# Optimization experiments

Hardware: AMD Instinct MI355X
Metric: run time of the kernel (lower is better)

Reference implementation:

```python
import jax, jax.numpy as jnp
import numpy as np

D_MODEL = 1024
NHEAD = 16
D_HEAD = D_MODEL // NHEAD


def setup_inputs() -> dict:
    key = jax.random.key(0)
    ks = jax.random.split(key, 5)
    s_in = 1.0 / np.sqrt(D_MODEL)
    x = jax.random.normal(ks[0], (2, 2048, D_MODEL), dtype=jnp.float32)
    Wqkv = jax.random.uniform(ks[1], (D_MODEL, 3 * D_MODEL), jnp.float32, -s_in, s_in)
    bqkv = jax.random.uniform(ks[2], (3 * D_MODEL,), jnp.float32, -s_in, s_in)
    Wproj = jax.random.uniform(ks[3], (D_MODEL, D_MODEL), jnp.float32, -s_in, s_in)
    bproj = jax.random.uniform(ks[4], (D_MODEL,), jnp.float32, -s_in, s_in)
    return {"x": x, "Wqkv": Wqkv, "bqkv": bqkv, "Wproj": Wproj, "bproj": bproj}


def reference(x, Wqkv, bqkv, Wproj, bproj):
    B, N, D = x.shape
    qkv = x @ Wqkv + bqkv                       # [B, N, 3D]
    q, k, v = jnp.split(qkv, 3, axis=-1)
    # [B, N, D] -> [B, H, N, d]
    def to_heads(t):
        return t.reshape(B, N, NHEAD, D_HEAD).transpose(0, 2, 1, 3)
    q, k, v = to_heads(q), to_heads(k), to_heads(v)
    scale = 1.0 / np.sqrt(D_HEAD).astype(np.float32)
    attn = jnp.einsum('bhqd,bhkd->bhqk', q, k) * scale
    attn = jax.nn.softmax(attn, axis=-1)
    y = jnp.einsum('bhqk,bhkd->bhqd', attn, v)  # [B, H, N, d]
    y = y.transpose(0, 2, 1, 3).reshape(B, N, D)
    return y @ Wproj + bproj
```

## Files before the change

kernel.cpp:

```cpp
#include <hip/hip_runtime.h>
#include <hip/hip_bf16.h>
#include <stdint.h>

typedef __hip_bfloat16 bf16;
typedef __attribute__((ext_vector_type(8))) short short8;
typedef __attribute__((ext_vector_type(4))) float f32x4;

#define QSCALE 0.18033688011f

__device__ __forceinline__ float fast_exp2(float x) {
#if __has_builtin(__builtin_amdgcn_exp2f)
  return __builtin_amdgcn_exp2f(x);
#else
  return exp2f(x);
#endif
}

__device__ __forceinline__ uint32_t pack2_bf16(float a, float b) {
#if __has_builtin(__builtin_amdgcn_cvt_pk_bf16_f32)
  typedef __attribute__((ext_vector_type(2))) __bf16 bf16x2;
  bf16x2 v = __builtin_amdgcn_cvt_pk_bf16_f32(a, b);
  return __builtin_bit_cast(uint32_t, v);
#else
  uint32_t ua = __builtin_bit_cast(uint32_t, a);
  uint32_t ub = __builtin_bit_cast(uint32_t, b);
  ua += 0x7FFF + ((ua >> 16) & 1);
  ub += 0x7FFF + ((ub >> 16) & 1);
  return (ua >> 16) | (ub & 0xFFFF0000u);
#endif
}

__device__ __forceinline__ void gload_lds16(const bf16* g, bf16* l) {
#if __has_builtin(__builtin_amdgcn_global_load_lds)
  __builtin_amdgcn_global_load_lds(
      (const __attribute__((address_space(1))) void*)(uintptr_t)g,
      (__attribute__((address_space(3))) void*)(uint32_t)(uintptr_t)l,
      16, 0, 0);
#else
  int lane = threadIdx.x & 63;
  *(short8*)(l + lane * 8) = *(const short8*)(g + lane * 8);
#endif
}

__device__ __forceinline__ void lds_barrier() {
  asm volatile("s_waitcnt lgkmcnt(0)\n\ts_barrier" ::: "memory");
}

__device__ __forceinline__ void transpose_tile(const float* __restrict__ in,
                                               bf16* __restrict__ out,
                                               int R, int C, int bx, int by,
                                               bf16 (*t)[72]) {
  const int r0 = by * 64, c0 = bx * 64;
  const int rr = threadIdx.x >> 3, cc = (threadIdx.x & 7) * 8;
#pragma unroll
  for (int rep = 0; rep < 2; ++rep) {
    int y = rr + rep * 32;
    const float* p = in + (size_t)(r0 + y) * C + c0 + cc;
    f32x4 v0 = *(const f32x4*)p;
    f32x4 v1 = *(const f32x4*)(p + 4);
#pragma unroll
    for (int j = 0; j < 4; ++j) {
      t[cc + j][y] = __float2bfloat16(v0[j]);
      t[cc + 4 + j][y] = __float2bfloat16(v1[j]);
    }
  }
  __syncthreads();
#pragma unroll
  for (int rep = 0; rep < 2; ++rep) {
    int y = rr + rep * 32;
    short8 v = *(const short8*)&t[y][cc];
    *(short8*)(out + (size_t)(c0 + y) * R + r0 + cc) = v;
  }
}

__global__ __launch_bounds__(256)
void prep_k(const float* __restrict__ x, bf16* __restrict__ xb,
            const float* __restrict__ Wqkv, bf16* __restrict__ WtQkv,
            const float* __restrict__ Wproj, bf16* __restrict__ WtP) {
  __shared__ __align__(16) bf16 t[64][72];
  const int bid = blockIdx.x;
  if (bid < 2048) {
    int i = (bid * 256 + threadIdx.x) * 8;
    f32x4 v0 = *(const f32x4*)(x + i);
    f32x4 v1 = *(const f32x4*)(x + i + 4);
    short8 r;
    bf16* rb = (bf16*)&r;
#pragma unroll
    for (int j = 0; j < 4; ++j) {
      rb[j] = __float2bfloat16(v0[j]);
      rb[4 + j] = __float2bfloat16(v1[j]);
    }
    *(short8*)(xb + i) = r;
  } else if (bid < 2048 + 768) {
    int b = bid - 2048;
    transpose_tile(Wqkv, WtQkv, 1024, 3072, b % 48, b / 48, t);
  } else {
    int b = bid - 2816;
    transpose_tile(Wproj, WtP, 1024, 1024, b % 16, b / 16, t);
  }
}

template <int MODE, int TM>
__global__ __launch_bounds__(256, 2)
void gemm_bt(const bf16* __restrict__ A, const bf16* __restrict__ Bt,
             const float* __restrict__ bias, float* __restrict__ outp,
             bf16* __restrict__ Qd, bf16* __restrict__ Kd, bf16* __restrict__ Vt,
             int M, int Nn, int K) {
  constexpr int MI = TM / 32;
  __shared__ __align__(16) bf16 smem[(TM == 128) ? 9216 : 6144];
  bf16* As = smem;
  bf16* Bs = smem + TM * 32;

  const int tid = threadIdx.x;
  const int wave = tid >> 6, lane = tid & 63;
  const int quad = lane >> 4, l16 = lane & 15;
  const int mw = (wave >> 1) * (TM / 2), nw = (wave & 1) * 64;
  const int m_blk = blockIdx.y * TM, n_blk = blockIdx.x * 128;

  f32x4 acc[MI][4];
#pragma unroll
  for (int i = 0; i < MI; ++i)
#pragma unroll
    for (int j = 0; j < 4; ++j) acc[i][j] = (f32x4){0.f, 0.f, 0.f, 0.f};

  const int rowA = lane >> 2, colA = (lane & 3) * 8;
  const int chunkB = wave * 2;
  const bf16* gB = Bt + (size_t)(n_blk + chunkB * 16 + rowA) * K + colA;
  bf16* lB0 = &Bs[chunkB * 16 * 32];
  bf16* lB1 = &Bs[(chunkB + 1) * 16 * 32];

  const int chunkA = (TM == 128) ? wave * 2 : wave;
  const bf16* gA = A + (size_t)(m_blk + chunkA * 16 + rowA) * K + colA;
  bf16* lA0 = &As[chunkA * 16 * 32];
  bf16* lA1 = &As[(chunkA + 1) * 16 * 32];

  for (int kt = 0; kt < K; kt += 32) {
    gload_lds16(gA, lA0);
    if (TM == 128) gload_lds16(gA + 16 * K, lA1);
    gload_lds16(gB, lB0);
    gload_lds16(gB + 16 * K, lB1);
    gA += 32; gB += 32;
    __syncthreads();
    short8 af[MI], bfv[4];
#pragma unroll
    for (int i = 0; i < MI; ++i)
      af[i] = *(const short8*)&As[(mw + i * 16 + l16) * 32 + quad * 8];
#pragma unroll
    for (int j = 0; j < 4; ++j)
      bfv[j] = *(const short8*)&Bs[(nw + j * 16 + l16) * 32 + quad * 8];
#pragma unroll
    for (int i = 0; i < MI; ++i)
#pragma unroll
      for (int j = 0; j < 4; ++j)
        acc[i][j] = __builtin_amdgcn_mfma_f32_16x16x32_bf16(af[i], bfv[j],
                                                            acc[i][j], 0, 0, 0);
    __syncthreads();
  }

  if (MODE == 0) {
    float bval[4];
#pragma unroll
    for (int j = 0; j < 4; ++j) bval[j] = bias[n_blk + nw + j * 16 + l16];

    const int part = n_blk >> 10;
    const int b = m_blk >> 11;
    const int tloc = m_blk & 2047;
    const int h0 = (n_blk & 1023) >> 6;

#pragma unroll
    for (int p = 0; p < 2; ++p) {
      __syncthreads();
      if ((nw >> 6) == p) {
        if (part == 2) {
#pragma unroll
          for (int i = 0; i < MI; ++i)
#pragma unroll
            for (int j = 0; j < 4; ++j) {
              const int dh = j * 16 + l16;
              const int t0 = mw + i * 16 + quad * 4;
              uint2 pk;
              pk.x = pack2_bf16(acc[i][j][0] + bval[j], acc[i][j][1] + bval[j]);
              pk.y = pack2_bf16(acc[i][j][2] + bval[j], acc[i][j][3] + bval[j]);
              *(uint2*)&smem[dh * 136 + t0] = pk;
            }
        } else {
          const float sc = (part == 0) ? QSCALE : 1.0f;
#pragma unroll
          for (int i = 0; i < MI; ++i)
#pragma unroll
            for (int j = 0; j < 4; ++j) {
              const int d = j * 16 + l16;
              const int t0 = mw + i * 16 + quad * 4;
#pragma unroll
              for (int r = 0; r < 4; ++r)
                smem[(t0 + r) * 72 + d] =
                    __float2bfloat16((acc[i][j][r] + bval[j]) * sc);
            }
        }
      }
      __syncthreads();
      const size_t bh = (size_t)(b * 16 + h0 + p);
      if (part == 2) {
#pragma unroll
        for (int it = 0; it < 4; ++it) {
          const int dl = (tid >> 4) + it * 16;
          const int t8 = (tid & 15) * 8;
          short8 v = *(const short8*)&smem[dl * 136 + t8];
          *(short8*)&Vt[(bh * 64 + dl) * 2048 + tloc + t8] = v;
        }
      } else {
        bf16* dst = (part == 0) ? Qd : Kd;
#pragma unroll
        for (int it = 0; it < 4; ++it) {
          const int row = (tid >> 3) + it * 32;
          const int col8 = (tid & 7) * 8;
          short8 v = *(const short8*)&smem[row * 72 + col8];
          *(short8*)&dst[(bh * 2048 + tloc + row) * 64 + col8] = v;
        }
      }
    }
  } else {
#pragma unroll
    for (int j = 0; j < 4; ++j) {
      const int ncol = n_blk + nw + j * 16 + l16;
      const float bval = bias[ncol];
#pragma unroll
      for (int i = 0; i < MI; ++i) {
        const int mrow0 = m_blk + mw + i * 16 + quad * 4;
#pragma unroll
        for (int r = 0; r < 4; ++r)
          outp[(size_t)(mrow0 + r) * Nn + ncol] = acc[i][j][r] + bval;
      }
    }
  }
}

__global__ __launch_bounds__(256, 4)
void attn_kernel(const bf16* __restrict__ Qg, const bf16* __restrict__ Kg,
                 const bf16* __restrict__ Vt, bf16* __restrict__ yg) {
  __shared__ __align__(16) bf16 Ks[64][72];
  __shared__ __align__(16) bf16 Vts[2][64 * 72];
  __shared__ __align__(16) bf16 Ps[64][72];

  const int tid = threadIdx.x;
  const int wave = tid >> 6, lane = tid & 63;
  const int quad = lane >> 4, l16 = lane & 15;
  const int qh = wave & 1, kvh = wave >> 1;

  const int bx = blockIdx.x;
  const int qt = bx & 31;
  const int bh = bx >> 5;

  const bf16* Qb = Qg + ((size_t)bh * 2048 + qt * 64) * 64;
  const bf16* Kb = Kg + (size_t)bh * 2048 * 64;
  const bf16* Vtb = Vt + (size_t)bh * 64 * 2048;

  short8 qf[2][2];
#pragma unroll
  for (int qblk = 0; qblk < 2; ++qblk)
#pragma unroll
    for (int kb = 0; kb < 2; ++kb)
      qf[qblk][kb] = *(const short8*)(
          Qb + (size_t)(qh * 32 + qblk * 16 + l16) * 64 + kb * 32 + quad * 8);

  f32x4 yacc[2][4];
#pragma unroll
  for (int qblk = 0; qblk < 2; ++qblk)
#pragma unroll
    for (int dblk = 0; dblk < 4; ++dblk)
      yacc[qblk][dblk] = (f32x4){0.f, 0.f, 0.f, 0.f};
  float sum_l[2] = {0.f, 0.f};

  const int kr = tid >> 3, kc = (tid & 7) * 8;
  const int vdd = tid & 63, vo = tid >> 6;
  const int voff0 = vdd * 72 + (((vo) + (vdd >> 3)) & 7) * 8;
  const int voff1 = vdd * 72 + (((vo + 4) + (vdd >> 3)) & 7) * 8;
  const bf16* Kp0 = Kb + (size_t)kr * 64 + kc;
  const bf16* Kp1 = Kb + (size_t)(kr + 32) * 64 + kc;
  const bf16* Vp0 = Vtb + (size_t)vdd * 2048 + vo * 8;
  const bf16* Vp1 = Vtb + (size_t)vdd * 2048 + (vo + 4) * 8;

  {
    short8 a = *(const short8*)Kp0;
    short8 b = *(const short8*)Kp1;
    short8 c = *(const short8*)Vp0;
    short8 d = *(const short8*)Vp1;
    *(short8*)&Ks[kr][kc] = a;
    *(short8*)&Ks[kr + 32][kc] = b;
    *(short8*)&Vts[0][voff0] = c;
    *(short8*)&Vts[0][voff1] = d;
  }
  short8 gk0 = *(const short8*)(Kp0 + (size_t)64 * 64);
  short8 gk1 = *(const short8*)(Kp1 + (size_t)64 * 64);
  short8 gv0 = *(const short8*)(Vp0 + 64);
  short8 gv1 = *(const short8*)(Vp1 + 64);
  __syncthreads();

  for (int kt = 0; kt < 2048; kt += 64) {
    const int cur = (kt >> 6) & 1;

    if (kt + 64 < 2048) {
      *(short8*)&Vts[cur ^ 1][voff0] = gv0;
      *(short8*)&Vts[cur ^ 1][voff1] = gv1;
      if (kt + 128 < 2048) {
        gv0 = *(const short8*)(Vp0 + kt + 128);
        gv1 = *(const short8*)(Vp1 + kt + 128);
      }
    }

    f32x4 st[2][2];
#pragma unroll
    for (int kvblk = 0; kvblk < 2; ++kvblk) {
      const int krow = kvh * 32 + kvblk * 16 + l16;
      short8 kf0 = *(const short8*)&Ks[krow][quad * 8];
      short8 kf1 = *(const short8*)&Ks[krow][32 + quad * 8];
#pragma unroll
      for (int qblk = 0; qblk < 2; ++qblk) {
        f32x4 a = (f32x4){0.f, 0.f, 0.f, 0.f};
        a = __builtin_amdgcn_mfma_f32_16x16x32_bf16(kf0, qf[qblk][0], a, 0, 0, 0);
        a = __builtin_amdgcn_mfma_f32_16x16x32_bf16(kf1, qf[qblk][1], a, 0, 0, 0);
        st[qblk][kvblk] = a;
      }
    }

#pragma unroll
    for (int qblk = 0; qblk < 2; ++qblk) {
      float ssum = 0.f;
#pragma unroll
      for (int kvblk = 0; kvblk < 2; ++kvblk) {
        float p0 = fast_exp2(st[qblk][kvblk][0]);
        float p1 = fast_exp2(st[qblk][kvblk][1]);
        float p2 = fast_exp2(st[qblk][kvblk][2]);
        float p3 = fast_exp2(st[qblk][kvblk][3]);
        ssum += (p0 + p1) + (p2 + p3);
        uint2 pk;
        pk.x = pack2_bf16(p0, p1);
        pk.y = pack2_bf16(p2, p3);
        *(uint2*)&Ps[qh * 32 + qblk * 16 + l16]
                    [kvh * 32 + kvblk * 16 + quad * 4] = pk;
      }
      sum_l[qblk] += ssum;
    }

    lds_barrier();

    if (kt + 64 < 2048) {
      *(short8*)&Ks[kr][kc] = gk0;
      *(short8*)&Ks[kr + 32][kc] = gk1;
      if (kt + 128 < 2048) {
        gk0 = *(const short8*)(Kp0 + (size_t)(kt + 128) * 64);
        gk1 = *(const short8*)(Kp1 + (size_t)(kt + 128) * 64);
      }
    }

    short8 vbf[4];
#pragma unroll
    for (int dblk = 0; dblk < 4; ++dblk) {
      const int d = dblk * 16 + l16;
      vbf[dblk] = *(const short8*)&Vts[cur][d * 72 +
          (((kvh * 4 + quad) + (d >> 3)) & 7) * 8];
    }
#pragma unroll
    for (int qblk = 0; qblk < 2; ++qblk) {
      short8 pa = *(const short8*)&Ps[qh * 32 + qblk * 16 + l16]
                                     [kvh * 32 + quad * 8];
#pragma unroll
      for (int dblk = 0; dblk < 4; ++dblk)
        yacc[qblk][dblk] = __builtin_amdgcn_mfma_f32_16x16x32_bf16(
            pa, vbf[dblk], yacc[qblk][dblk], 0, 0, 0);
    }

    lds_barrier();
  }

#pragma unroll
  for (int qblk = 0; qblk < 2; ++qblk) {
    sum_l[qblk] += __shfl_xor(sum_l[qblk], 16);
    sum_l[qblk] += __shfl_xor(sum_l[qblk], 32);
  }
  __syncthreads();
  float* red = (float*)&Vts[0][0];
  float* sred = (float*)&Ps[0][0];
  if (kvh == 1) {
#pragma unroll
    for (int qblk = 0; qblk < 2; ++qblk) {
#pragma unroll
      for (int dblk = 0; dblk < 4; ++dblk) {
        const int f = (qh * 2 + qblk) * 4 + dblk;
        *(f32x4*)&red[(f * 64 + quad * 16 + l16) * 4] = yacc[qblk][dblk];
      }
      if (quad == 0) sred[(qh * 2 + qblk) * 16 + l16] = sum_l[qblk];
    }
  }
  __syncthreads();
  if (kvh == 0) {
    const int b = bh >> 4, h = bh & 15;
    const size_t rowbase = (size_t)b * 2048 + qt * 64;
#pragma unroll
    for (int qblk = 0; qblk < 2; ++qblk) {
      sum_l[qblk] += sred[(qh * 2 + qblk) * 16 + l16];
#pragma unroll
      for (int dblk = 0; dblk < 4; ++dblk) {
        const int f = (qh * 2 + qblk) * 4 + dblk;
        f32x4 o = *(const f32x4*)&red[(f * 64 + quad * 16 + l16) * 4];
#pragma unroll
        for (int r = 0; r < 4; ++r) yacc[qblk][dblk][r] += o[r];
      }
#pragma unroll
      for (int r = 0; r < 4; ++r) {
        const float lv = __shfl(sum_l[qblk], quad * 4 + r, 16);
        const float inv = 1.f / lv;
        const int rr = qh * 32 + qblk * 16 + quad * 4 + r;
#pragma unroll
        for (int dblk = 0; dblk < 4; ++dblk)
          yg[(rowbase + rr) * 1024 + h * 64 + dblk * 16 + l16] =
              __float2bfloat16(yacc[qblk][dblk][r] * inv);
      }
    }
  }
}

extern "C" void kernel_launch(void* const* d_in, const int* in_sizes, int n_in,
                              void* d_out, int out_size, void* d_ws, size_t ws_size,
                              hipStream_t stream) {
  const float* x = (const float*)d_in[0];
  const float* Wqkv = (const float*)d_in[1];
  const float* bqkv = (const float*)d_in[2];
  const float* Wproj = (const float*)d_in[3];
  const float* bproj = (const float*)d_in[4];
  float* out = (float*)d_out;

  if (ws_size < (size_t)40 * 1024 * 1024) return;

  char* ws = (char*)d_ws;
  bf16* xb    = (bf16*)(ws + 0);
  bf16* yd    = (bf16*)(ws + 0);
  bf16* WtQkv = (bf16*)(ws + 8388608);
  bf16* WtP   = (bf16*)(ws + 14680064);
  bf16* Qd    = (bf16*)(ws + 16777216);
  bf16* Kd    = (bf16*)(ws + 25165824);
  bf16* Vten  = (bf16*)(ws + 33554432);

  prep_k<<<3072, 256, 0, stream>>>(x, xb, Wqkv, WtQkv, Wproj, WtP);
  gemm_bt<0, 128><<<dim3(24, 32), 256, 0, stream>>>(
      xb, WtQkv, bqkv, nullptr, Qd, Kd, Vten, 4096, 3072, 1024);
  attn_kernel<<<dim3(1024), 256, 0, stream>>>(Qd, Kd, Vten, yd);
  gemm_bt<1, 64><<<dim3(8, 64), 256, 0, stream>>>(
      yd, WtP, bproj, out, nullptr, nullptr, nullptr, 4096, 1024, 1024);
}
```

Measured before the change: 193.6 us.

## Load K/V MFMA fragments directly from global into registers, dropping LDS staging

```diff
diff --git a/kernel.cpp b/kernel.cpp
--- a/kernel.cpp
+++ b/kernel.cpp
@@ -42,10 +42,6 @@
 #endif
 }
 
-__device__ __forceinline__ void lds_barrier() {
-  asm volatile("s_waitcnt lgkmcnt(0)\n\ts_barrier" ::: "memory");
-}
-
 __device__ __forceinline__ void transpose_tile(const float* __restrict__ in,
                                                bf16* __restrict__ out,
                                                int R, int C, int bx, int by,
@@ -238,9 +234,8 @@
 __global__ __launch_bounds__(256, 4)
 void attn_kernel(const bf16* __restrict__ Qg, const bf16* __restrict__ Kg,
                  const bf16* __restrict__ Vt, bf16* __restrict__ yg) {
-  __shared__ __align__(16) bf16 Ks[64][72];
-  __shared__ __align__(16) bf16 Vts[2][64 * 72];
-  __shared__ __align__(16) bf16 Ps[64][72];
+  __shared__ __align__(16) char lds_pool[16640];
+  bf16 (*Ps)[72] = (bf16 (*)[72])lds_pool;
 
   const int tid = threadIdx.x;
   const int wave = tid >> 6, lane = tid & 63;
@@ -252,8 +247,8 @@
   const int bh = bx >> 5;
 
   const bf16* Qb = Qg + ((size_t)bh * 2048 + qt * 64) * 64;
-  const bf16* Kb = Kg + (size_t)bh * 2048 * 64;
-  const bf16* Vtb = Vt + (size_t)bh * 64 * 2048;
+  const bf16* kp = Kg + ((size_t)bh * 2048 + kvh * 32 + l16) * 64 + quad * 8;
+  const bf16* vp = Vt + ((size_t)bh * 64 + l16) * 2048 + kvh * 32 + quad * 8;
 
   short8 qf[2][2];
 #pragma unroll
@@ -263,6 +258,16 @@
       qf[qblk][kb] = *(const short8*)(
           Qb + (size_t)(qh * 32 + qblk * 16 + l16) * 64 + kb * 32 + quad * 8);
 
+  short8 kf[2][2], vf[4];
+#pragma unroll
+  for (int kvblk = 0; kvblk < 2; ++kvblk)
+#pragma unroll
+    for (int ks = 0; ks < 2; ++ks)
+      kf[kvblk][ks] = *(const short8*)(kp + kvblk * 1024 + ks * 32);
+#pragma unroll
+  for (int dblk = 0; dblk < 4; ++dblk)
+    vf[dblk] = *(const short8*)(vp + (size_t)dblk * 16 * 2048);
+
   f32x4 yacc[2][4];
 #pragma unroll
   for (int qblk = 0; qblk < 2; ++qblk)
@@ -271,56 +276,27 @@
       yacc[qblk][dblk] = (f32x4){0.f, 0.f, 0.f, 0.f};
   float sum_l[2] = {0.f, 0.f};
 
-  const int kr = tid >> 3, kc = (tid & 7) * 8;
-  const int vdd = tid & 63, vo = tid >> 6;
-  const int voff0 = vdd * 72 + (((vo) + (vdd >> 3)) & 7) * 8;
-  const int voff1 = vdd * 72 + (((vo + 4) + (vdd >> 3)) & 7) * 8;
-  const bf16* Kp0 = Kb + (size_t)kr * 64 + kc;
-  const bf16* Kp1 = Kb + (size_t)(kr + 32) * 64 + kc;
-  const bf16* Vp0 = Vtb + (size_t)vdd * 2048 + vo * 8;
-  const bf16* Vp1 = Vtb + (size_t)vdd * 2048 + (vo + 4) * 8;
-
-  {
-    short8 a = *(const short8*)Kp0;
-    short8 b = *(const short8*)Kp1;
-    short8 c = *(const short8*)Vp0;
-    short8 d = *(const short8*)Vp1;
-    *(short8*)&Ks[kr][kc] = a;
-    *(short8*)&Ks[kr + 32][kc] = b;
-    *(short8*)&Vts[0][voff0] = c;
-    *(short8*)&Vts[0][voff1] = d;
-  }
-  short8 gk0 = *(const short8*)(Kp0 + (size_t)64 * 64);
-  short8 gk1 = *(const short8*)(Kp1 + (size_t)64 * 64);
-  short8 gv0 = *(const short8*)(Vp0 + 64);
-  short8 gv1 = *(const short8*)(Vp1 + 64);
-  __syncthreads();
-
   for (int kt = 0; kt < 2048; kt += 64) {
-    const int cur = (kt >> 6) & 1;
-
-    if (kt + 64 < 2048) {
-      *(short8*)&Vts[cur ^ 1][voff0] = gv0;
-      *(short8*)&Vts[cur ^ 1][voff1] = gv1;
-      if (kt + 128 < 2048) {
-        gv0 = *(const short8*)(Vp0 + kt + 128);
-        gv1 = *(const short8*)(Vp1 + kt + 128);
-      }
-    }
-
     f32x4 st[2][2];
 #pragma unroll
-    for (int kvblk = 0; kvblk < 2; ++kvblk) {
-      const int krow = kvh * 32 + kvblk * 16 + l16;
-      short8 kf0 = *(const short8*)&Ks[krow][quad * 8];
-      short8 kf1 = *(const short8*)&Ks[krow][32 + quad * 8];
+    for (int kvblk = 0; kvblk < 2; ++kvblk)
 #pragma unroll
       for (int qblk = 0; qblk < 2; ++qblk) {
         f32x4 a = (f32x4){0.f, 0.f, 0.f, 0.f};
-        a = __builtin_amdgcn_mfma_f32_16x16x32_bf16(kf0, qf[qblk][0], a, 0, 0, 0);
-        a = __builtin_amdgcn_mfma_f32_16x16x32_bf16(kf1, qf[qblk][1], a, 0, 0, 0);
+        a = __builtin_amdgcn_mfma_f32_16x16x32_bf16(kf[kvblk][0], qf[qblk][0],
+                                                    a, 0, 0, 0);
+        a = __builtin_amdgcn_mfma_f32_16x16x32_bf16(kf[kvblk][1], qf[qblk][1],
+                                                    a, 0, 0, 0);
         st[qblk][kvblk] = a;
       }
+
+    if (kt + 64 < 2048) {
+      kp += 64 * 64;
+#pragma unroll
+      for (int kvblk = 0; kvblk < 2; ++kvblk)
+#pragma unroll
+        for (int ks = 0; ks < 2; ++ks)
+          kf[kvblk][ks] = *(const short8*)(kp + kvblk * 1024 + ks * 32);
     }
 
 #pragma unroll
@@ -342,24 +318,6 @@
       sum_l[qblk] += ssum;
     }
 
-    lds_barrier();
-
-    if (kt + 64 < 2048) {
-      *(short8*)&Ks[kr][kc] = gk0;
-      *(short8*)&Ks[kr + 32][kc] = gk1;
-      if (kt + 128 < 2048) {
-        gk0 = *(const short8*)(Kp0 + (size_t)(kt + 128) * 64);
-        gk1 = *(const short8*)(Kp1 + (size_t)(kt + 128) * 64);
-      }
-    }
-
-    short8 vbf[4];
-#pragma unroll
-    for (int dblk = 0; dblk < 4; ++dblk) {
-      const int d = dblk * 16 + l16;
-      vbf[dblk] = *(const short8*)&Vts[cur][d * 72 +
-          (((kvh * 4 + quad) + (d >> 3)) & 7) * 8];
-    }
 #pragma unroll
     for (int qblk = 0; qblk < 2; ++qblk) {
       short8 pa = *(const short8*)&Ps[qh * 32 + qblk * 16 + l16]
@@ -367,10 +325,15 @@
 #pragma unroll
       for (int dblk = 0; dblk < 4; ++dblk)
         yacc[qblk][dblk] = __builtin_amdgcn_mfma_f32_16x16x32_bf16(
-            pa, vbf[dblk], yacc[qblk][dblk], 0, 0, 0);
-    }
-
-    lds_barrier();
+            pa, vf[dblk], yacc[qblk][dblk], 0, 0, 0);
+    }
+
+    if (kt + 64 < 2048) {
+      vp += 64;
+#pragma unroll
+      for (int dblk = 0; dblk < 4; ++dblk)
+        vf[dblk] = *(const short8*)(vp + (size_t)dblk * 16 * 2048);
+    }
   }
 
 #pragma unroll
@@ -379,8 +342,8 @@
     sum_l[qblk] += __shfl_xor(sum_l[qblk], 32);
   }
   __syncthreads();
-  float* red = (float*)&Vts[0][0];
-  float* sred = (float*)&Ps[0][0];
+  float* red = (float*)lds_pool;
+  float* sred = (float*)(lds_pool + 16384);
   if (kvh == 1) {
 #pragma unroll
     for (int qblk = 0; qblk < 2; ++qblk) {
```

New measurement: 254.3 us. +31.3%, slower.

## Keep P in registers via 16x16x16 MFMA and split KV across all waves

Applied to the files above, without the earlier changes.

```diff
diff --git a/kernel.cpp b/kernel.cpp
--- a/kernel.cpp
+++ b/kernel.cpp
@@ -4,6 +4,7 @@
 
 typedef __hip_bfloat16 bf16;
 typedef __attribute__((ext_vector_type(8))) short short8;
+typedef __attribute__((ext_vector_type(4))) short s16x4;
 typedef __attribute__((ext_vector_type(4))) float f32x4;
 
 #define QSCALE 0.18033688011f
@@ -30,6 +31,20 @@
 #endif
 }
 
+#if __has_builtin(__builtin_amdgcn_mfma_f32_16x16x16bf16_1k)
+#define MFMA_PV(a, b, c) __builtin_amdgcn_mfma_f32_16x16x16bf16_1k(a, b, c, 0, 0, 0)
+#elif __has_builtin(__builtin_amdgcn_mfma_f32_16x16x16_bf16_1k)
+#define MFMA_PV(a, b, c) __builtin_amdgcn_mfma_f32_16x16x16_bf16_1k(a, b, c, 0, 0, 0)
+#else
+__device__ __forceinline__ f32x4 mfma_pv_asm(s16x4 a, s16x4 b, f32x4 c) {
+  f32x4 d;
+  asm("v_mfma_f32_16x16x16_bf16 %0, %1, %2, %3"
+      : "=&v"(d) : "v"(a), "v"(b), "v"(c));
+  return d;
+}
+#define MFMA_PV(a, b, c) mfma_pv_asm(a, b, c)
+#endif
+
 __device__ __forceinline__ void gload_lds16(const bf16* g, bf16* l) {
 #if __has_builtin(__builtin_amdgcn_global_load_lds)
   __builtin_amdgcn_global_load_lds(
@@ -235,17 +250,16 @@
   }
 }
 
-__global__ __launch_bounds__(256, 4)
+__global__ __launch_bounds__(256, 3)
 void attn_kernel(const bf16* __restrict__ Qg, const bf16* __restrict__ Kg,
                  const bf16* __restrict__ Vt, bf16* __restrict__ yg) {
-  __shared__ __align__(16) bf16 Ks[64][72];
-  __shared__ __align__(16) bf16 Vts[2][64 * 72];
-  __shared__ __align__(16) bf16 Ps[64][72];
+  __shared__ __align__(16) char pool[36864];
+  bf16* KsB = (bf16*)pool;
+  bf16* VtsB = (bf16*)(pool + 18432);
 
   const int tid = threadIdx.x;
   const int wave = tid >> 6, lane = tid & 63;
   const int quad = lane >> 4, l16 = lane & 15;
-  const int qh = wave & 1, kvh = wave >> 1;
 
   const int bx = blockIdx.x;
   const int qt = bx & 31;
@@ -255,21 +269,13 @@
   const bf16* Kb = Kg + (size_t)bh * 2048 * 64;
   const bf16* Vtb = Vt + (size_t)bh * 64 * 2048;
 
-  short8 qf[2][2];
-#pragma unroll
-  for (int qblk = 0; qblk < 2; ++qblk)
-#pragma unroll
-    for (int kb = 0; kb < 2; ++kb)
-      qf[qblk][kb] = *(const short8*)(
-          Qb + (size_t)(qh * 32 + qblk * 16 + l16) * 64 + kb * 32 + quad * 8);
-
-  f32x4 yacc[2][4];
-#pragma unroll
-  for (int qblk = 0; qblk < 2; ++qblk)
-#pragma unroll
-    for (int dblk = 0; dblk < 4; ++dblk)
-      yacc[qblk][dblk] = (f32x4){0.f, 0.f, 0.f, 0.f};
-  float sum_l[2] = {0.f, 0.f};
+  short8 qf[4][2];
+#pragma unroll
+  for (int qblk = 0; qblk < 4; ++qblk)
+#pragma unroll
+    for (int ks = 0; ks < 2; ++ks)
+      qf[qblk][ks] = *(const short8*)(
+          Qb + (size_t)(qblk * 16 + l16) * 64 + ks * 32 + quad * 8);
 
   const int kr = tid >> 3, kc = (tid & 7) * 8;
   const int vdd = tid & 63, vo = tid >> 6;
@@ -285,10 +291,10 @@
     short8 b = *(const short8*)Kp1;
     short8 c = *(const short8*)Vp0;
     short8 d = *(const short8*)Vp1;
-    *(short8*)&Ks[kr][kc] = a;
-    *(short8*)&Ks[kr + 32][kc] = b;
-    *(short8*)&Vts[0][voff0] = c;
-    *(short8*)&Vts[0][voff1] = d;
+    *(short8*)(KsB + kr * 72 + kc) = a;
+    *(short8*)(KsB + (kr + 32) * 72 + kc) = b;
+    *(short8*)(VtsB + voff0) = c;
+    *(short8*)(VtsB + voff1) = d;
   }
   short8 gk0 = *(const short8*)(Kp0 + (size_t)64 * 64);
   short8 gk1 = *(const short8*)(Kp1 + (size_t)64 * 64);
@@ -296,121 +302,137 @@
   short8 gv1 = *(const short8*)(Vp1 + 64);
   __syncthreads();
 
+  f32x4 yacc[4][4];
+#pragma unroll
+  for (int qblk = 0; qblk < 4; ++qblk)
+#pragma unroll
+    for (int dblk = 0; dblk < 4; ++dblk)
+      yacc[qblk][dblk] = (f32x4){0.f, 0.f, 0.f, 0.f};
+  float sum_l[4] = {0.f, 0.f, 0.f, 0.f};
+
+  const int kfo = (wave * 16 + l16) * 72 + quad * 8;
+  int vbo[4];
+#pragma unroll
+  for (int dblk = 0; dblk < 4; ++dblk) {
+    const int d = dblk * 16 + l16;
+    const int c = wave * 2 + (quad >> 1);
+    vbo[dblk] = d * 72 + ((c + (d >> 3)) & 7) * 8 + (quad & 1) * 4;
+  }
+
   for (int kt = 0; kt < 2048; kt += 64) {
     const int cur = (kt >> 6) & 1;
+    bf16* KsC = KsB + cur * 4608;
+    bf16* VtsC = VtsB + cur * 4608;
 
     if (kt + 64 < 2048) {
-      *(short8*)&Vts[cur ^ 1][voff0] = gv0;
-      *(short8*)&Vts[cur ^ 1][voff1] = gv1;
-      if (kt + 128 < 2048) {
-        gv0 = *(const short8*)(Vp0 + kt + 128);
-        gv1 = *(const short8*)(Vp1 + kt + 128);
-      }
-    }
-
-    f32x4 st[2][2];
-#pragma unroll
-    for (int kvblk = 0; kvblk < 2; ++kvblk) {
-      const int krow = kvh * 32 + kvblk * 16 + l16;
-      short8 kf0 = *(const short8*)&Ks[krow][quad * 8];
-      short8 kf1 = *(const short8*)&Ks[krow][32 + quad * 8];
-#pragma unroll
-      for (int qblk = 0; qblk < 2; ++qblk) {
-        f32x4 a = (f32x4){0.f, 0.f, 0.f, 0.f};
-        a = __builtin_amdgcn_mfma_f32_16x16x32_bf16(kf0, qf[qblk][0], a, 0, 0, 0);
-        a = __builtin_amdgcn_mfma_f32_16x16x32_bf16(kf1, qf[qblk][1], a, 0, 0, 0);
-        st[qblk][kvblk] = a;
-      }
-    }
-
-#pragma unroll
-    for (int qblk = 0; qblk < 2; ++qblk) {
-      float ssum = 0.f;
-#pragma unroll
-      for (int kvblk = 0; kvblk < 2; ++kvblk) {
-        float p0 = fast_exp2(st[qblk][kvblk][0]);
-        float p1 = fast_exp2(st[qblk][kvblk][1]);
-        float p2 = fast_exp2(st[qblk][kvblk][2]);
-        float p3 = fast_exp2(st[qblk][kvblk][3]);
-        ssum += (p0 + p1) + (p2 + p3);
-        uint2 pk;
-        pk.x = pack2_bf16(p0, p1);
-        pk.y = pack2_bf16(p2, p3);
-        *(uint2*)&Ps[qh * 32 + qblk * 16 + l16]
-                    [kvh * 32 + kvblk * 16 + quad * 4] = pk;
-      }
-      sum_l[qblk] += ssum;
-    }
-
-    lds_barrier();
-
-    if (kt + 64 < 2048) {
-      *(short8*)&Ks[kr][kc] = gk0;
-      *(short8*)&Ks[kr + 32][kc] = gk1;
+      bf16* KsN = KsB + (cur ^ 1) * 4608;
+      bf16* VtsN = VtsB + (cur ^ 1) * 4608;
+      *(short8*)(KsN + kr * 72 + kc) = gk0;
+      *(short8*)(KsN + (kr + 32) * 72 + kc) = gk1;
+      *(short8*)(VtsN + voff0) = gv0;
+      *(short8*)(VtsN + voff1) = gv1;
       if (kt + 128 < 2048) {
         gk0 = *(const short8*)(Kp0 + (size_t)(kt + 128) * 64);
         gk1 = *(const short8*)(Kp1 + (size_t)(kt + 128) * 64);
-      }
-    }
-
-    short8 vbf[4];
-#pragma unroll
-    for (int dblk = 0; dblk < 4; ++dblk) {
-      const int d = dblk * 16 + l16;
-      vbf[dblk] = *(const short8*)&Vts[cur][d * 72 +
-          (((kvh * 4 + quad) + (d >> 3)) & 7) * 8];
-    }
-#pragma unroll
-    for (int qblk = 0; qblk < 2; ++qblk) {
-      short8 pa = *(const short8*)&Ps[qh * 32 + qblk * 16 + l16]
-                                     [kvh * 32 + quad * 8];
+        gv0 = *(const short8*)(Vp0 + kt + 128);
+        gv1 = *(const short8*)(Vp1 + kt + 128);
+      }
+    }
+
+    short8 kf0 = *(const short8*)(KsC + kfo);
+    short8 kf1 = *(const short8*)(KsC + kfo + 32);
+    s16x4 vb[4];
+#pragma unroll
+    for (int dblk = 0; dblk < 4; ++dblk)
+      vb[dblk] = *(const s16x4*)(VtsC + vbo[dblk]);
+
+    s16x4 pa[4];
+#pragma unroll
+    for (int qblk = 0; qblk < 4; ++qblk) {
+      f32x4 a = (f32x4){0.f, 0.f, 0.f, 0.f};
+      a = __builtin_amdgcn_mfma_f32_16x16x32_bf16(kf0, qf[qblk][0], a, 0, 0, 0);
+      a = __builtin_amdgcn_mfma_f32_16x16x32_bf16(kf1, qf[qblk][1], a, 0, 0, 0);
+      float p0 = fast_exp2(a[0]);
+      float p1 = fast_exp2(a[1]);
+      float p2 = fast_exp2(a[2]);
+      float p3 = fast_exp2(a[3]);
+      sum_l[qblk] += (p0 + p1) + (p2 + p3);
+      uint2 pk;
+      pk.x = pack2_bf16(p0, p1);
+      pk.y = pack2_bf16(p2, p3);
+      pa[qblk] = __builtin_bit_cast(s16x4, pk);
+    }
+
+#pragma unroll
+    for (int qblk = 0; qblk < 4; ++qblk)
 #pragma unroll
       for (int dblk = 0; dblk < 4; ++dblk)
-        yacc[qblk][dblk] = __builtin_amdgcn_mfma_f32_16x16x32_bf16(
-            pa, vbf[dblk], yacc[qblk][dblk], 0, 0, 0);
-    }
+        yacc[qblk][dblk] = MFMA_PV(pa[qblk], vb[dblk], yacc[qblk][dblk]);
 
     lds_barrier();
   }
 
 #pragma unroll
-  for (int qblk = 0; qblk < 2; ++qblk) {
+  for (int qblk = 0; qblk < 4; ++qblk) {
     sum_l[qblk] += __shfl_xor(sum_l[qblk], 16);
     sum_l[qblk] += __shfl_xor(sum_l[qblk], 32);
   }
+  float* red = (float*)pool;
+  float* sred = (float*)(pool + 32768);
+  if (lane < 16) {
+#pragma unroll
+    for (int qblk = 0; qblk < 4; ++qblk)
+      sred[wave * 64 + qblk * 16 + l16] = sum_l[qblk];
+  }
+  if (wave & 1) {
+    float* buf = red + (wave >> 1) * 4096;
+#pragma unroll
+    for (int qblk = 0; qblk < 4; ++qblk)
+#pragma unroll
+      for (int dblk = 0; dblk < 4; ++dblk)
+        *(f32x4*)&buf[((qblk * 4 + dblk) * 64 + quad * 16 + l16) * 4] =
+            yacc[qblk][dblk];
+  }
   __syncthreads();
-  float* red = (float*)&Vts[0][0];
-  float* sred = (float*)&Ps[0][0];
-  if (kvh == 1) {
-#pragma unroll
-    for (int qblk = 0; qblk < 2; ++qblk) {
+  if (!(wave & 1)) {
+    float* buf = red + (wave >> 1) * 4096;
+#pragma unroll
+    for (int qblk = 0; qblk < 4; ++qblk)
 #pragma unroll
       for (int dblk = 0; dblk < 4; ++dblk) {
-        const int f = (qh * 2 + qblk) * 4 + dblk;
-        *(f32x4*)&red[(f * 64 + quad * 16 + l16) * 4] = yacc[qblk][dblk];
-      }
-      if (quad == 0) sred[(qh * 2 + qblk) * 16 + l16] = sum_l[qblk];
-    }
+        f32x4 o = *(const f32x4*)&buf[((qblk * 4 + dblk) * 64 + quad * 16 + l16) * 4];
+#pragma unroll
+        for (int r = 0; r < 4; ++r) yacc[qblk][dblk][r] += o[r];
+      }
   }
   __syncthreads();
-  if (kvh == 0) {
+  if (wave == 2) {
+#pragma unroll
+    for (int qblk = 0; qblk < 4; ++qblk)
+#pragma unroll
+      for (int dblk = 0; dblk < 4; ++dblk)
+        *(f32x4*)&red[((qblk * 4 + dblk) * 64 + quad * 16 + l16) * 4] =
+            yacc[qblk][dblk];
+  }
+  __syncthreads();
+  if (wave == 0) {
     const int b = bh >> 4, h = bh & 15;
     const size_t rowbase = (size_t)b * 2048 + qt * 64;
 #pragma unroll
-    for (int qblk = 0; qblk < 2; ++qblk) {
-      sum_l[qblk] += sred[(qh * 2 + qblk) * 16 + l16];
+    for (int qblk = 0; qblk < 4; ++qblk) {
+      float stot = sred[qblk * 16 + l16] + sred[64 + qblk * 16 + l16] +
+                   sred[128 + qblk * 16 + l16] + sred[192 + qblk * 16 + l16];
 #pragma unroll
       for (int dblk = 0; dblk < 4; ++dblk) {
-        const int f = (qh * 2 + qblk) * 4 + dblk;
-        f32x4 o = *(const f32x4*)&red[(f * 64 + quad * 16 + l16) * 4];
+        f32x4 o = *(const f32x4*)&red[((qblk * 4 + dblk) * 64 + quad * 16 + l16) * 4];
 #pragma unroll
         for (int r = 0; r < 4; ++r) yacc[qblk][dblk][r] += o[r];
       }
 #pragma unroll
       for (int r = 0; r < 4; ++r) {
-        const float lv = __shfl(sum_l[qblk], quad * 4 + r, 16);
+        const float lv = __shfl(stot, quad * 4 + r, 16);
         const float inv = 1.f / lv;
-        const int rr = qh * 32 + qblk * 16 + quad * 4 + r;
+        const int rr = qblk * 16 + quad * 4 + r;
 #pragma unroll
         for (int dblk = 0; dblk < 4; ++dblk)
           yg[(rowbase + rr) * 1024 + h * 64 + dblk * 16 + l16] =
```

Result: slower. 202.1 us (+4.4%).

## Keep softmax probabilities in registers and double-buffer K to drop a barrier

Applied to the files above, without the earlier changes.

```diff
diff --git a/kernel.cpp b/kernel.cpp
--- a/kernel.cpp
+++ b/kernel.cpp
@@ -238,9 +238,9 @@
 __global__ __launch_bounds__(256, 4)
 void attn_kernel(const bf16* __restrict__ Qg, const bf16* __restrict__ Kg,
                  const bf16* __restrict__ Vt, bf16* __restrict__ yg) {
-  __shared__ __align__(16) bf16 Ks[64][72];
-  __shared__ __align__(16) bf16 Vts[2][64 * 72];
-  __shared__ __align__(16) bf16 Ps[64][72];
+  __shared__ __align__(16) char pool[36864];
+  bf16* KsB = (bf16*)pool;
+  bf16* VtsB = (bf16*)(pool + 18432);
 
   const int tid = threadIdx.x;
   const int wave = tid >> 6, lane = tid & 63;
@@ -259,17 +259,9 @@
 #pragma unroll
   for (int qblk = 0; qblk < 2; ++qblk)
 #pragma unroll
-    for (int kb = 0; kb < 2; ++kb)
-      qf[qblk][kb] = *(const short8*)(
-          Qb + (size_t)(qh * 32 + qblk * 16 + l16) * 64 + kb * 32 + quad * 8);
-
-  f32x4 yacc[2][4];
-#pragma unroll
-  for (int qblk = 0; qblk < 2; ++qblk)
-#pragma unroll
-    for (int dblk = 0; dblk < 4; ++dblk)
-      yacc[qblk][dblk] = (f32x4){0.f, 0.f, 0.f, 0.f};
-  float sum_l[2] = {0.f, 0.f};
+    for (int ks = 0; ks < 2; ++ks)
+      qf[qblk][ks] = *(const short8*)(
+          Qb + (size_t)(qh * 32 + qblk * 16 + l16) * 64 + ks * 32 + quad * 8);
 
   const int kr = tid >> 3, kc = (tid & 7) * 8;
   const int vdd = tid & 63, vo = tid >> 6;
@@ -285,10 +277,10 @@
     short8 b = *(const short8*)Kp1;
     short8 c = *(const short8*)Vp0;
     short8 d = *(const short8*)Vp1;
-    *(short8*)&Ks[kr][kc] = a;
-    *(short8*)&Ks[kr + 32][kc] = b;
-    *(short8*)&Vts[0][voff0] = c;
-    *(short8*)&Vts[0][voff1] = d;
+    *(short8*)(KsB + kr * 72 + kc) = a;
+    *(short8*)(KsB + (kr + 32) * 72 + kc) = b;
+    *(short8*)(VtsB + voff0) = c;
+    *(short8*)(VtsB + voff1) = d;
   }
   short8 gk0 = *(const short8*)(Kp0 + (size_t)64 * 64);
   short8 gk1 = *(const short8*)(Kp1 + (size_t)64 * 64);
@@ -296,78 +288,87 @@
   short8 gv1 = *(const short8*)(Vp1 + 64);
   __syncthreads();
 
+  f32x4 yacc[2][4];
+#pragma unroll
+  for (int qblk = 0; qblk < 2; ++qblk)
+#pragma unroll
+    for (int dblk = 0; dblk < 4; ++dblk)
+      yacc[qblk][dblk] = (f32x4){0.f, 0.f, 0.f, 0.f};
+  float sum_l[2] = {0.f, 0.f};
+
+  const int kfo = (kvh * 32 + l16) * 72 + quad * 8;
+  int vbo[4][2];
+#pragma unroll
+  for (int dblk = 0; dblk < 4; ++dblk) {
+    const int d = dblk * 16 + l16;
+#pragma unroll
+    for (int kvblk = 0; kvblk < 2; ++kvblk) {
+      const int c = kvh * 4 + kvblk * 2 + (quad >> 1);
+      vbo[dblk][kvblk] = d * 72 + ((c + (d >> 3)) & 7) * 8 + (quad & 1) * 4;
+    }
+  }
+
   for (int kt = 0; kt < 2048; kt += 64) {
     const int cur = (kt >> 6) & 1;
+    bf16* KsC = KsB + cur * 4608;
+    bf16* VtsC = VtsB + cur * 4608;
 
     if (kt + 64 < 2048) {
-      *(short8*)&Vts[cur ^ 1][voff0] = gv0;
-      *(short8*)&Vts[cur ^ 1][voff1] = gv1;
-      if (kt + 128 < 2048) {
-        gv0 = *(const short8*)(Vp0 + kt + 128);
-        gv1 = *(const short8*)(Vp1 + kt + 128);
-      }
-    }
-
-    f32x4 st[2][2];
-#pragma unroll
-    for (int kvblk = 0; kvblk < 2; ++kvblk) {
-      const int krow = kvh * 32 + kvblk * 16 + l16;
-      short8 kf0 = *(const short8*)&Ks[krow][quad * 8];
-      short8 kf1 = *(const short8*)&Ks[krow][32 + quad * 8];
-#pragma unroll
-      for (int qblk = 0; qblk < 2; ++qblk) {
-        f32x4 a = (f32x4){0.f, 0.f, 0.f, 0.f};
-        a = __builtin_amdgcn_mfma_f32_16x16x32_bf16(kf0, qf[qblk][0], a, 0, 0, 0);
-        a = __builtin_amdgcn_mfma_f32_16x16x32_bf16(kf1, qf[qblk][1], a, 0, 0, 0);
-        st[qblk][kvblk] = a;
-      }
-    }
-
-#pragma unroll
-    for (int qblk = 0; qblk < 2; ++qblk) {
-      float ssum = 0.f;
-#pragma unroll
-      for (int kvblk = 0; kvblk < 2; ++kvblk) {
-        float p0 = fast_exp2(st[qblk][kvblk][0]);
-        float p1 = fast_exp2(st[qblk][kvblk][1]);
-        float p2 = fast_exp2(st[qblk][kvblk][2]);
-        float p3 = fast_exp2(st[qblk][kvblk][3]);
-        ssum += (p0 + p1) + (p2 + p3);
-        uint2 pk;
-        pk.x = pack2_bf16(p0, p1);
-        pk.y = pack2_bf16(p2, p3);
-        *(uint2*)&Ps[qh * 32 + qblk * 16 + l16]
-                    [kvh * 32 + kvblk * 16 + quad * 4] = pk;
-      }
-      sum_l[qblk] += ssum;
-    }
-
-    lds_barrier();
-
-    if (kt + 64 < 2048) {
-      *(short8*)&Ks[kr][kc] = gk0;
-      *(short8*)&Ks[kr + 32][kc] = gk1;
+      bf16* KsN = KsB + (cur ^ 1) * 4608;
+      bf16* VtsN = VtsB + (cur ^ 1) * 4608;
+      *(short8*)(KsN + kr * 72 + kc) = gk0;
+      *(short8*)(KsN + (kr + 32) * 72 + kc) = gk1;
+      *(short8*)(VtsN + voff0) = gv0;
+      *(short8*)(VtsN + voff1) = gv1;
       if (kt + 128 < 2048) {
         gk0 = *(const short8*)(Kp0 + (size_t)(kt + 128) * 64);
         gk1 = *(const short8*)(Kp1 + (size_t)(kt + 128) * 64);
-      }
-    }
-
-    short8 vbf[4];
+        gv0 = *(const short8*)(Vp0 + kt + 128);
+        gv1 = *(const short8*)(Vp1 + kt + 128);
+      }
+    }
+
+    short8 kf[2][2];
+#pragma unroll
+    for (int kvblk = 0; kvblk < 2; ++kvblk)
+#pragma unroll
+      for (int ks = 0; ks < 2; ++ks)
+        kf[kvblk][ks] =
+            *(const short8*)(KsC + kfo + kvblk * 16 * 72 + ks * 32);
+
+    short8 pa8[2];
+#pragma unroll
+    for (int qblk = 0; qblk < 2; ++qblk) {
+      f32x4 s0 = (f32x4){0.f, 0.f, 0.f, 0.f};
+      f32x4 s1 = (f32x4){0.f, 0.f, 0.f, 0.f};
+      s0 = __builtin_amdgcn_mfma_f32_16x16x32_bf16(kf[0][0], qf[qblk][0], s0, 0, 0, 0);
+      s0 = __builtin_amdgcn_mfma_f32_16x16x32_bf16(kf[0][1], qf[qblk][1], s0, 0, 0, 0);
+      s1 = __builtin_amdgcn_mfma_f32_16x16x32_bf16(kf[1][0], qf[qblk][0], s1, 0, 0, 0);
+      s1 = __builtin_amdgcn_mfma_f32_16x16x32_bf16(kf[1][1], qf[qblk][1], s1, 0, 0, 0);
+      float p0 = fast_exp2(s0[0]), p1 = fast_exp2(s0[1]);
+      float p2 = fast_exp2(s0[2]), p3 = fast_exp2(s0[3]);
+      float p4 = fast_exp2(s1[0]), p5 = fast_exp2(s1[1]);
+      float p6 = fast_exp2(s1[2]), p7 = fast_exp2(s1[3]);
+      sum_l[qblk] += ((p0 + p1) + (p2 + p3)) + ((p4 + p5) + (p6 + p7));
+      uint4 u;
+      u.x = pack2_bf16(p0, p1);
+      u.y = pack2_bf16(p2, p3);
+      u.z = pack2_bf16(p4, p5);
+      u.w = pack2_bf16(p6, p7);
+      pa8[qblk] = __builtin_bit_cast(short8, u);
+    }
+
 #pragma unroll
     for (int dblk = 0; dblk < 4; ++dblk) {
-      const int d = dblk * 16 + l16;
-      vbf[dblk] = *(const short8*)&Vts[cur][d * 72 +
-          (((kvh * 4 + quad) + (d >> 3)) & 7) * 8];
-    }
-#pragma unroll
-    for (int qblk = 0; qblk < 2; ++qblk) {
-      short8 pa = *(const short8*)&Ps[qh * 32 + qblk * 16 + l16]
-                                     [kvh * 32 + quad * 8];
-#pragma unroll
-      for (int dblk = 0; dblk < 4; ++dblk)
-        yacc[qblk][dblk] = __builtin_amdgcn_mfma_f32_16x16x32_bf16(
-            pa, vbf[dblk], yacc[qblk][dblk], 0, 0, 0);
+      uint2 lo = *(const uint2*)(VtsC + vbo[dblk][0]);
+      uint2 hi = *(const uint2*)(VtsC + vbo[dblk][1]);
+      uint4 u;
+      u.x = lo.x; u.y = lo.y; u.z = hi.x; u.w = hi.y;
+      short8 vb8 = __builtin_bit_cast(short8, u);
+      yacc[0][dblk] = __builtin_amdgcn_mfma_f32_16x16x32_bf16(
+          pa8[0], vb8, yacc[0][dblk], 0, 0, 0);
+      yacc[1][dblk] = __builtin_amdgcn_mfma_f32_16x16x32_bf16(
+          pa8[1], vb8, yacc[1][dblk], 0, 0, 0);
     }
 
     lds_barrier();
@@ -379,8 +380,8 @@
     sum_l[qblk] += __shfl_xor(sum_l[qblk], 32);
   }
   __syncthreads();
-  float* red = (float*)&Vts[0][0];
-  float* sred = (float*)&Ps[0][0];
+  float* red = (float*)pool;
+  float* sred = (float*)(pool + 16384);
   if (kvh == 1) {
 #pragma unroll
     for (int qblk = 0; qblk < 2; ++qblk) {
```

New measurement: 194.8 us. No clear change (+0.6%).
